# Optimization experiments

Measured on AMD Instinct MI355X. Metric: run time of the kernel, lower is better.

The kernel has to match this reference:

```python
import jax, jax.numpy as jnp
import numpy as np

WS = 7   # window_size
NH = 4   # num_head
EPS = 1e-5

def _rel_idx(ws):
    c = np.stack(np.meshgrid(np.arange(ws), np.arange(ws), indexing='ij')).reshape(2, -1)
    r = (c[:, :, None] - c[:, None, :]).transpose(1, 2, 0)
    r[..., 0] += ws - 1
    r[..., 1] += ws - 1
    r[..., 0] *= 2 * ws - 1
    return r.sum(-1)  # (ws^2, ws^2) int

def _shift_mask(ws, ps):
    # faithful to torch get_shift_mask: additive mask value is (1-eq)*1e-9 (as in source)
    wn = ps // ws
    ss = ws // 2
    rt = (np.arange(ps) + ss) // ws
    m = rt[:, None] * (ps // ws) + rt[None, :] + 1
    m = np.roll(m, (-ss, -ss), axis=(0, 1))
    m = m.reshape(wn, ws, wn, ws).transpose(0, 2, 1, 3).reshape(wn * wn, ws * ws)
    eq = (m[:, :, None] == m[:, None, :]).astype(np.float32)
    return (1.0 - eq) * 1e-9  # (num_windows, ws^2, ws^2)

def _ln(x, g, b):
    mu = x.mean(-1, keepdims=True)
    v = ((x - mu) ** 2).mean(-1, keepdims=True)
    return (x - mu) * jax.lax.rsqrt(v + EPS) * g + b

def _win_attn(x, wqkv, bqkv, wo, bo, table, mask):
    bs, S, D = x.shape
    hd = D // NH
    qkv = x @ wqkv.T + bqkv
    q, k, v = jnp.split(qkv, 3, axis=-1)
    def heads(t):
        return t.reshape(bs, S, NH, hd).transpose(0, 2, 1, 3).reshape(bs * NH, S, hd)
    q, k, v = heads(q), heads(k), heads(v)
    ridx = _rel_idx(WS).reshape(-1)
    bias = table[ridx].reshape(S, S, NH).transpose(2, 0, 1)  # (NH, S, S)
    scores = jnp.einsum('bqd,bkd->bqk', q, k) / np.sqrt(hd).astype(np.float32)
    scores = scores + jnp.tile(bias, (bs, 1, 1))
    if mask is not None:
        # source tiles mask head-major while q/k/v are batch-major; replicate faithfully
        scores = scores + jnp.tile(mask, (NH, 1, 1))
    p = jax.nn.softmax(scores, axis=-1)
    out = jnp.einsum('bqk,bkd->bqd', p, v)
    out = out.reshape(bs, NH, S, hd).transpose(0, 2, 1, 3).reshape(bs, S, D)
    return out @ wo.T + bo

def _forward(x, ln1_g, ln1_b, w_qkv1, b_qkv1, w_o1, b_o1, tbl1,
             ln2_g, ln2_b, w_mlp1, b_mlp1,
             ln3_g, ln3_b, w_qkv2, b_qkv2, w_o2, b_o2, tbl2,
             ln4_g, ln4_b, w_mlp2, b_mlp2):
    B, S, D = x.shape
    ps = int(np.sqrt(S))
    wn = ps // WS
    nw = wn * wn
    s2 = WS * WS
    ss = WS // 2
    # block 1: W-MSA (note: source's image2sequence is a plain reshape, no inverse transpose)
    y = _ln(x, ln1_g, ln1_b)
    y = y.reshape(B, wn, WS, wn, WS, D).transpose(0, 1, 3, 2, 4, 5).reshape(B * nw, s2, D)
    y = _win_attn(y, w_qkv1, b_qkv1, w_o1, b_o1, tbl1, None)
    y = y.reshape(B, S, D)
    x = x + y
    # mlp1
    y = _ln(x, ln2_g, ln2_b) @ w_mlp1.T + b_mlp1
    x = x + y
    # block 2: SW-MSA
    y = _ln(x, ln3_g, ln3_b)
    y = jnp.roll(y.reshape(B, ps, ps, D), (-ss, -ss), axis=(1, 2))
    y = y.reshape(B, wn, WS, wn, WS, D).transpose(0, 1, 3, 2, 4, 5).reshape(B * nw, s2, D)
    mask = jnp.tile(jnp.asarray(_shift_mask(WS, ps)), (B, 1, 1))
    y = _win_attn(y, w_qkv2, b_qkv2, w_o2, b_o2, tbl2, mask)
    y = y.reshape(B, wn, wn, WS, WS, D).transpose(0, 1, 3, 2, 4, 5).reshape(B, ps, ps, D)
    y = jnp.roll(y, (ss, ss), axis=(1, 2)).reshape(B, S, D)
    x = x + y
    # mlp2; source line `y + x + y` has no assignment, so the final residual is dropped
    y = _ln(x, ln4_g, ln4_b) @ w_mlp2.T + b_mlp2
    return y

def setup_inputs() -> dict:
    key = jax.random.key(0)
    ks = jax.random.split(key, 16)
    B, S, D = 64, 3136, 128
    T = (2 * WS - 1) ** 2  # 169
    f32 = jnp.float32
    inp = {
        'x': jax.random.normal(ks[0], (B, S, D), dtype=f32),
        'ln1_g': jnp.ones((D,), f32), 'ln1_b': jnp.zeros((D,), f32),
        'w_qkv1': jax.random.normal(ks[1], (3 * D, D), dtype=f32) * 0.02,
        'b_qkv1': jnp.zeros((3 * D,), f32),
        'w_o1': jax.random.normal(ks[2], (D, D), dtype=f32) * 0.02,
        'b_o1': jnp.zeros((D,), f32),
        'tbl1': jax.random.normal(ks[3], (T, NH), dtype=f32) * 0.02,
        'ln2_g': jnp.ones((D,), f32), 'ln2_b': jnp.zeros((D,), f32),
        'w_mlp1': jax.random.normal(ks[4], (D, D), dtype=f32) * 0.02,
        'b_mlp1': jnp.zeros((D,), f32),
        'ln3_g': jnp.ones((D,), f32), 'ln3_b': jnp.zeros((D,), f32),
        'w_qkv2': jax.random.normal(ks[5], (3 * D, D), dtype=f32) * 0.02,
        'b_qkv2': jnp.zeros((3 * D,), f32),
        'w_o2': jax.random.normal(ks[6], (D, D), dtype=f32) * 0.02,
        'b_o2': jnp.zeros((D,), f32),
        'tbl2': jax.random.normal(ks[7], (T, NH), dtype=f32) * 0.02,
        'ln4_g': jnp.ones((D,), f32), 'ln4_b': jnp.zeros((D,), f32),
        'w_mlp2': jax.random.normal(ks[8], (D, D), dtype=f32) * 0.02,
        'b_mlp2': jnp.zeros((D,), f32),
    }
    return inp

def reference(x, ln1_g, ln1_b, w_qkv1, b_qkv1, w_o1, b_o1, tbl1,
              ln2_g, ln2_b, w_mlp1, b_mlp1,
              ln3_g, ln3_b, w_qkv2, b_qkv2, w_o2, b_o2, tbl2,
              ln4_g, ln4_b, w_mlp2, b_mlp2):
    return _forward(x, ln1_g, ln1_b, w_qkv1, b_qkv1, w_o1, b_o1, tbl1,
                    ln2_g, ln2_b, w_mlp1, b_mlp1,
                    ln3_g, ln3_b, w_qkv2, b_qkv2, w_o2, b_o2, tbl2,
                    ln4_g, ln4_b, w_mlp2, b_mlp2)
```

## Files before the change

### kernel.cpp

```cpp
#include <hip/hip_runtime.h>
#include <hip/hip_bf16.h>
#include <stdint.h>

#define PS 56
#define S_ 3136
#define DIM 128
#define NTOK 200704

typedef __attribute__((ext_vector_type(8))) short short8;
typedef __attribute__((ext_vector_type(4))) float f32x4;

__device__ __forceinline__ uint32_t bfpack(float a, float b){
  uint32_t ua = __float_as_uint(a); ua = (ua + 0x7fffu + ((ua >> 16) & 1u)) >> 16;
  uint32_t ub = __float_as_uint(b); ub = (ub + 0x7fffu + ((ub >> 16) & 1u)) & 0xffff0000u;
  return ua | ub;
}
__device__ __forceinline__ uint16_t bf16of(float a){
  uint32_t ua = __float_as_uint(a);
  return (uint16_t)((ua + 0x7fffu + ((ua >> 16) & 1u)) >> 16);
}
__device__ __forceinline__ int rr(int row){ return row > 48 ? 49 : row; }

__device__ __forceinline__ int win_map(int r, int shift) {
  int b = r / S_;
  int rem = r - b * S_;
  int w = rem / 49;
  int p = rem - w * 49;
  int i = p / 7, j = p - i * 7;
  int wr = w >> 3, wc = w & 7;
  int row = wr * 7 + i + shift; if (row >= PS) row -= PS;
  int col = wc * 7 + j + shift; if (col >= PS) col -= PS;
  return b * S_ + row * PS + col;
}

__global__ __launch_bounds__(256) void ln_k(const float* __restrict__ X,
                                            const float* __restrict__ g,
                                            const float* __restrict__ b,
                                            uint16_t* __restrict__ O) {
  int t = blockIdx.x * 4 + (threadIdx.x >> 6);
  int lane = threadIdx.x & 63;
  float2 v = *(const float2*)(X + (size_t)t * DIM + lane * 2);
  float s = v.x + v.y, sq = v.x * v.x + v.y * v.y;
  #pragma unroll
  for (int o = 32; o; o >>= 1) { s += __shfl_xor(s, o); sq += __shfl_xor(sq, o); }
  float mu = s * (1.0f / 128.0f);
  float rs = rsqrtf(sq * (1.0f / 128.0f) - mu * mu + 1e-5f);
  float2 gg = *(const float2*)(g + lane * 2);
  float2 bb = *(const float2*)(b + lane * 2);
  float a = (v.x - mu) * rs * gg.x + bb.x;
  float c = (v.y - mu) * rs * gg.y + bb.y;
  ((uint32_t*)O)[(size_t)t * 64 + lane] = bfpack(a, c);
}

__global__ __launch_bounds__(256) void wconv_k(
    const float* __restrict__ w0, const float* __restrict__ w1,
    const float* __restrict__ w2, const float* __restrict__ w3,
    const float* __restrict__ w4, const float* __restrict__ w5,
    uint16_t* __restrict__ out) {
  int i = blockIdx.x * 256 + threadIdx.x;
  float v;
  if      (i <  49152) v = w0[i];
  else if (i <  98304) v = w1[i -  49152];
  else if (i < 114688) v = w2[i -  98304];
  else if (i < 131072) v = w3[i - 114688];
  else if (i < 147456) v = w4[i - 131072];
  else                 v = w5[i - 147456];
  out[i] = bf16of(v);
}

__global__ __launch_bounds__(256) void bias_k(const float* __restrict__ tbl, float* __restrict__ biasT) {
  int idx = blockIdx.x * 256 + threadIdx.x;
  int h = idx >> 12;
  int k = (idx >> 6) & 63;
  int q = idx & 63;
  float v;
  if (k >= 49)      v = -1e30f;
  else if (q >= 49) v = 0.f;
  else {
    int yi = q / 7, xi = q - yi * 7;
    int yj = k / 7, xj = k - yj * 7;
    v = tbl[((yi - yj + 6) * 13 + (xi - xj + 6)) * 4 + h];
  }
  biasT[idx] = v;
}

constexpr int QKV_STR = 392;
constexpr int OS_STR  = 140;

template<int IN_SHIFT, int OUT_SHIFT, bool MLP_LN>
__global__ __launch_bounds__(256) void attn4(const uint16_t* __restrict__ xbin,
                                             const uint16_t* __restrict__ Wqkv,
                                             const float* __restrict__ bqkv,
                                             const float* __restrict__ biasT,
                                             const uint16_t* __restrict__ Wo,
                                             const float* __restrict__ bo,
                                             const float* __restrict__ Rsrc,
                                             const uint16_t* __restrict__ Wm,
                                             const float* __restrict__ bm,
                                             const float* __restrict__ lnga,
                                             const float* __restrict__ lnba,
                                             const float* __restrict__ lngp,
                                             const float* __restrict__ lnbp,
                                             float* __restrict__ Xout,
                                             uint16_t* __restrict__ xbout)
{
  __shared__ __align__(16) uint16_t qs[50 * QKV_STR];
  __shared__ float lnred[50][4][2];
  const int tid = threadIdx.x;
  const int lane = tid & 63;
  const int h = tid >> 6;
  const int lanelow = lane & 15;
  const int quad = lane >> 4;
  const int base = blockIdx.x * 49;

  {
    short8 af[4][4];
    #pragma unroll
    for (int mt = 0; mt < 4; ++mt) {
      int tok = mt * 16 + lanelow; if (tok > 48) tok = 48;
      int src = win_map(base + tok, IN_SHIFT);
      const uint16_t* arow = xbin + (size_t)src * DIM;
      #pragma unroll
      for (int k0 = 0; k0 < 4; ++k0)
        af[mt][k0] = *(const short8*)(arow + k0 * 32 + quad * 8);
    }
    #pragma unroll
    for (int ntl = 0; ntl < 6; ++ntl) {
      int wrow = (ntl >> 1) * 128 + h * 32 + (ntl & 1) * 16 + lanelow;
      const uint16_t* wr_ = Wqkv + (size_t)wrow * DIM;
      short8 bfr[4];
      #pragma unroll
      for (int k0 = 0; k0 < 4; ++k0)
        bfr[k0] = *(const short8*)(wr_ + k0 * 32 + quad * 8);
      f32x4 a4[4];
      #pragma unroll
      for (int mt = 0; mt < 4; ++mt) a4[mt] = (f32x4){0.f, 0.f, 0.f, 0.f};
      __builtin_amdgcn_s_setprio(1);
      #pragma unroll
      for (int k0 = 0; k0 < 4; ++k0)
        #pragma unroll
        for (int mt = 0; mt < 4; ++mt)
          a4[mt] = __builtin_amdgcn_mfma_f32_16x16x32_bf16(af[mt][k0], bfr[k0], a4[mt], 0, 0, 0);
      __builtin_amdgcn_s_setprio(0);
      float bq = bqkv[wrow];
      #pragma unroll
      for (int mt = 0; mt < 4; ++mt)
        #pragma unroll
        for (int r = 0; r < 4; ++r)
          qs[rr(mt * 16 + quad * 4 + r) * QKV_STR + wrow] = bf16of(a4[mt][r] + bq);
    }
  }

  const int n0 = h * 32 + lanelow, n1 = n0 + 16;
  int   orow_a[4][4];
  float r0a[4][4], r1a[4][4];
  #pragma unroll
  for (int qt = 0; qt < 4; ++qt)
    #pragma unroll
    for (int r = 0; r < 4; ++r) {
      int q = qt * 16 + quad * 4 + r;
      bool ok = (q < 49);
      int wrow = base + (ok ? q : 0);
      int orow = (OUT_SHIFT < 0) ? wrow : win_map(wrow, OUT_SHIFT);
      orow_a[qt][r] = orow;
      r0a[qt][r] = ok ? Rsrc[(size_t)orow * DIM + n0] : 0.f;
      r1a[qt][r] = ok ? Rsrc[(size_t)orow * DIM + n1] : 0.f;
    }

  f32x4 sc[4][4];
  #pragma unroll
  for (int kt = 0; kt < 4; ++kt)
    #pragma unroll
    for (int qt = 0; qt < 4; ++qt) sc[kt][qt] = (f32x4){0.f, 0.f, 0.f, 0.f};
  {
    short8 kf[4], qf[4];
    const int kcol = 128 + h * 32 + quad * 8;
    const int qcol = h * 32 + quad * 8;
    #pragma unroll
    for (int t = 0; t < 4; ++t) {
      int tok = t * 16 + lanelow; if (tok > 48) tok = 48;
      kf[t] = *(const short8*)(qs + tok * QKV_STR + kcol);
      qf[t] = *(const short8*)(qs + tok * QKV_STR + qcol);
    }
    __syncthreads();
    __builtin_amdgcn_s_setprio(1);
    #pragma unroll
    for (int kt = 0; kt < 4; ++kt)
      #pragma unroll
      for (int qt = 0; qt < 4; ++qt)
        sc[kt][qt] = __builtin_amdgcn_mfma_f32_16x16x32_bf16(kf[kt], qf[qt], sc[kt][qt], 0, 0, 0);
    __builtin_amdgcn_s_setprio(0);
  }

  const float* bh = biasT + h * 4096;
  #pragma unroll
  for (int kt = 0; kt < 4; ++kt)
    #pragma unroll
    for (int r = 0; r < 4; ++r) {
      const float* br = bh + (kt * 16 + quad * 4 + r) * 64 + lanelow;
      #pragma unroll
      for (int qt = 0; qt < 4; ++qt)
        sc[kt][qt][r] = fmaf(sc[kt][qt][r], 0.17677669529663689f, br[qt * 16]);
    }
  #pragma unroll
  for (int qt = 0; qt < 4; ++qt) {
    float m = sc[0][qt][0];
    #pragma unroll
    for (int kt = 0; kt < 4; ++kt)
      #pragma unroll
      for (int r = 0; r < 4; ++r) m = fmaxf(m, sc[kt][qt][r]);
    m = fmaxf(m, __shfl_xor(m, 16));
    m = fmaxf(m, __shfl_xor(m, 32));
    float s = 0.f;
    #pragma unroll
    for (int kt = 0; kt < 4; ++kt)
      #pragma unroll
      for (int r = 0; r < 4; ++r) {
        float e = __expf(sc[kt][qt][r] - m);
        sc[kt][qt][r] = e;
        s += e;
      }
    s += __shfl_xor(s, 16);
    s += __shfl_xor(s, 32);
    float inv = 1.0f / s;
    #pragma unroll
    for (int kt = 0; kt < 4; ++kt)
      #pragma unroll
      for (int r = 0; r < 4; ++r) sc[kt][qt][r] *= inv;
  }

  uint16_t* pw = qs + h * 64;
  #pragma unroll
  for (int qt = 0; qt < 4; ++qt)
    #pragma unroll
    for (int kt = 0; kt < 4; ++kt) {
      uint2 pk;
      pk.x = bfpack(sc[kt][qt][0], sc[kt][qt][1]);
      pk.y = bfpack(sc[kt][qt][2], sc[kt][qt][3]);
      *(uint2*)(pw + rr(qt * 16 + lanelow) * QKV_STR + kt * 16 + quad * 4) = pk;
    }

  f32x4 oc[4][2];
  #pragma unroll
  for (int qt = 0; qt < 4; ++qt)
    #pragma unroll
    for (int dt = 0; dt < 2; ++dt) oc[qt][dt] = (f32x4){0.f, 0.f, 0.f, 0.f};
  {
    short8 pf[4][2];
    #pragma unroll
    for (int qt = 0; qt < 4; ++qt)
      #pragma unroll
      for (int kp = 0; kp < 2; ++kp)
        pf[qt][kp] = *(const short8*)(pw + rr(qt * 16 + lanelow) * QKV_STR + kp * 32 + quad * 8);
    short8 vf[2][2];
    #pragma unroll
    for (int dt = 0; dt < 2; ++dt)
      #pragma unroll
      for (int kp = 0; kp < 2; ++kp) {
        short8 b;
        #pragma unroll
        for (int j = 0; j < 8; ++j) {
          int tok = kp * 32 + quad * 8 + j; if (tok > 48) tok = 48;
          b[j] = (short)qs[tok * QKV_STR + 256 + h * 32 + dt * 16 + lanelow];
        }
        vf[dt][kp] = b;
      }
    __builtin_amdgcn_s_setprio(1);
    #pragma unroll
    for (int qt = 0; qt < 4; ++qt)
      #pragma unroll
      for (int dt = 0; dt < 2; ++dt)
        #pragma unroll
        for (int kp = 0; kp < 2; ++kp)
          oc[qt][dt] = __builtin_amdgcn_mfma_f32_16x16x32_bf16(pf[qt][kp], vf[dt][kp], oc[qt][dt], 0, 0, 0);
    __builtin_amdgcn_s_setprio(0);
  }

  __syncthreads();
  uint16_t* Os = qs;
  #pragma unroll
  for (int qt = 0; qt < 4; ++qt)
    #pragma unroll
    for (int r = 0; r < 4; ++r) {
      int t = qt * 16 + quad * 4 + r;
      #pragma unroll
      for (int dt = 0; dt < 2; ++dt)
        Os[t * OS_STR + h * 32 + dt * 16 + lanelow] = bf16of(oc[qt][dt][r]);
    }
  __syncthreads();

  f32x4 rc[4][2];
  #pragma unroll
  for (int qt = 0; qt < 4; ++qt)
    #pragma unroll
    for (int dt = 0; dt < 2; ++dt) rc[qt][dt] = (f32x4){0.f, 0.f, 0.f, 0.f};
  #pragma unroll
  for (int kp = 0; kp < 4; ++kp) {
    short8 af[4];
    #pragma unroll
    for (int qt = 0; qt < 4; ++qt)
      af[qt] = *(const short8*)&Os[(qt * 16 + lanelow) * OS_STR + kp * 32 + quad * 8];
    short8 bfr[2];
    #pragma unroll
    for (int dt = 0; dt < 2; ++dt)
      bfr[dt] = *(const short8*)(Wo + (size_t)(h * 32 + dt * 16 + lanelow) * DIM + kp * 32 + quad * 8);
    __builtin_amdgcn_s_setprio(1);
    #pragma unroll
    for (int qt = 0; qt < 4; ++qt)
      #pragma unroll
      for (int dt = 0; dt < 2; ++dt)
        rc[qt][dt] = __builtin_amdgcn_mfma_f32_16x16x32_bf16(af[qt], bfr[dt], rc[qt][dt], 0, 0, 0);
    __builtin_amdgcn_s_setprio(0);
  }

  const float b0 = bo[n0], b1 = bo[n1];
  const float ga0 = lnga[n0], ga1 = lnga[n1];
  const float ea0 = lnba[n0], ea1 = lnba[n1];
  #pragma unroll
  for (int qt = 0; qt < 4; ++qt)
    #pragma unroll
    for (int r = 0; r < 4; ++r) {
      int q = qt * 16 + quad * 4 + r;
      float v0 = rc[qt][0][r] + b0 + r0a[qt][r];
      float v1 = rc[qt][1][r] + b1 + r1a[qt][r];
      rc[qt][0][r] = v0; rc[qt][1][r] = v1;
      float s = v0 + v1, sq = v0 * v0 + v1 * v1;
      s += __shfl_xor(s, 1); sq += __shfl_xor(sq, 1);
      s += __shfl_xor(s, 2); sq += __shfl_xor(sq, 2);
      s += __shfl_xor(s, 4); sq += __shfl_xor(sq, 4);
      s += __shfl_xor(s, 8); sq += __shfl_xor(sq, 8);
      if (lanelow == 0) { lnred[rr(q)][h][0] = s; lnred[rr(q)][h][1] = sq; }
    }
  __syncthreads();

  uint16_t* Xl = qs;
  #pragma unroll
  for (int qt = 0; qt < 4; ++qt)
    #pragma unroll
    for (int r = 0; r < 4; ++r) {
      int q = qt * 16 + quad * 4 + r;
      int ql = rr(q);
      float s  = lnred[ql][0][0] + lnred[ql][1][0] + lnred[ql][2][0] + lnred[ql][3][0];
      float sq = lnred[ql][0][1] + lnred[ql][1][1] + lnred[ql][2][1] + lnred[ql][3][1];
      float mu = s * (1.0f / 128.0f);
      float rs = rsqrtf(sq * (1.0f / 128.0f) - mu * mu + 1e-5f);
      Xl[q * OS_STR + n0] = bf16of((rc[qt][0][r] - mu) * rs * ga0 + ea0);
      Xl[q * OS_STR + n1] = bf16of((rc[qt][1][r] - mu) * rs * ga1 + ea1);
    }
  __syncthreads();

  f32x4 mc[4][2];
  #pragma unroll
  for (int qt = 0; qt < 4; ++qt)
    #pragma unroll
    for (int dt = 0; dt < 2; ++dt) mc[qt][dt] = (f32x4){0.f, 0.f, 0.f, 0.f};
  #pragma unroll
  for (int kp = 0; kp < 4; ++kp) {
    short8 af2[4];
    #pragma unroll
    for (int qt = 0; qt < 4; ++qt)
      af2[qt] = *(const short8*)&Xl[(qt * 16 + lanelow) * OS_STR + kp * 32 + quad * 8];
    short8 wfr[2];
    wfr[0] = *(const short8*)(Wm + (size_t)n0 * DIM + kp * 32 + quad * 8);
    wfr[1] = *(const short8*)(Wm + (size_t)n1 * DIM + kp * 32 + quad * 8);
    __builtin_amdgcn_s_setprio(1);
    #pragma unroll
    for (int qt = 0; qt < 4; ++qt)
      #pragma unroll
      for (int dt = 0; dt < 2; ++dt)
        mc[qt][dt] = __builtin_amdgcn_mfma_f32_16x16x32_bf16(af2[qt], wfr[dt], mc[qt][dt], 0, 0, 0);
    __builtin_amdgcn_s_setprio(0);
  }
  const float bm0 = bm[n0], bm1 = bm[n1];

  if constexpr (MLP_LN) {
    const float gp0 = lngp[n0], gp1 = lngp[n1];
    const float ep0 = lnbp[n0], ep1 = lnbp[n1];
    #pragma unroll
    for (int qt = 0; qt < 4; ++qt)
      #pragma unroll
      for (int r = 0; r < 4; ++r) {
        int q = qt * 16 + quad * 4 + r;
        float v0 = rc[qt][0][r] + mc[qt][0][r] + bm0;
        float v1 = rc[qt][1][r] + mc[qt][1][r] + bm1;
        rc[qt][0][r] = v0; rc[qt][1][r] = v1;
        float s = v0 + v1, sq = v0 * v0 + v1 * v1;
        s += __shfl_xor(s, 1); sq += __shfl_xor(sq, 1);
        s += __shfl_xor(s, 2); sq += __shfl_xor(sq, 2);
        s += __shfl_xor(s, 4); sq += __shfl_xor(sq, 4);
        s += __shfl_xor(s, 8); sq += __shfl_xor(sq, 8);
        if (lanelow == 0) { lnred[rr(q)][h][0] = s; lnred[rr(q)][h][1] = sq; }
      }
    __syncthreads();
    #pragma unroll
    for (int qt = 0; qt < 4; ++qt)
      #pragma unroll
      for (int r = 0; r < 4; ++r) {
        int q = qt * 16 + quad * 4 + r;
        if (q < 49) {
          int orow = orow_a[qt][r];
          float s  = lnred[q][0][0] + lnred[q][1][0] + lnred[q][2][0] + lnred[q][3][0];
          float sq = lnred[q][0][1] + lnred[q][1][1] + lnred[q][2][1] + lnred[q][3][1];
          float mu = s * (1.0f / 128.0f);
          float rs = rsqrtf(sq * (1.0f / 128.0f) - mu * mu + 1e-5f);
          float v0 = rc[qt][0][r], v1 = rc[qt][1][r];
          Xout[(size_t)orow * DIM + n0] = v0;
          Xout[(size_t)orow * DIM + n1] = v1;
          xbout[(size_t)orow * DIM + n0] = bf16of((v0 - mu) * rs * gp0 + ep0);
          xbout[(size_t)orow * DIM + n1] = bf16of((v1 - mu) * rs * gp1 + ep1);
        }
      }
  } else {
    #pragma unroll
    for (int qt = 0; qt < 4; ++qt)
      #pragma unroll
      for (int r = 0; r < 4; ++r) {
        int q = qt * 16 + quad * 4 + r;
        if (q < 49) {
          int orow = orow_a[qt][r];
          Xout[(size_t)orow * DIM + n0] = mc[qt][0][r] + bm0;
          Xout[(size_t)orow * DIM + n1] = mc[qt][1][r] + bm1;
        }
      }
  }
}

extern "C" void kernel_launch(void* const* d_in, const int* in_sizes, int n_in,
                              void* d_out, int out_size, void* d_ws, size_t ws_size,
                              hipStream_t stream) {
  const float* x0    = (const float*)d_in[0];
  const float* ln1g  = (const float*)d_in[1];
  const float* ln1b  = (const float*)d_in[2];
  const float* wqkv1 = (const float*)d_in[3];
  const float* bqkv1 = (const float*)d_in[4];
  const float* wo1   = (const float*)d_in[5];
  const float* bo1   = (const float*)d_in[6];
  const float* tbl1  = (const float*)d_in[7];
  const float* ln2g  = (const float*)d_in[8];
  const float* ln2b  = (const float*)d_in[9];
  const float* wm1   = (const float*)d_in[10];
  const float* bm1   = (const float*)d_in[11];
  const float* ln3g  = (const float*)d_in[12];
  const float* ln3b  = (const float*)d_in[13];
  const float* wqkv2 = (const float*)d_in[14];
  const float* bqkv2 = (const float*)d_in[15];
  const float* wo2   = (const float*)d_in[16];
  const float* bo2   = (const float*)d_in[17];
  const float* tbl2  = (const float*)d_in[18];
  const float* ln4g  = (const float*)d_in[19];
  const float* ln4b  = (const float*)d_in[20];
  const float* wm2   = (const float*)d_in[21];
  const float* bm2   = (const float*)d_in[22];

  char* ws = (char*)d_ws;
  size_t off = 0;
  uint16_t* xbA  = (uint16_t*)(ws + off); off += (size_t)NTOK * 128 * sizeof(uint16_t);
  uint16_t* xb2  = (uint16_t*)(ws + off); off += (size_t)NTOK * 128 * sizeof(uint16_t);
  float* biasT1  = (float*)(ws + off);    off += 16384 * sizeof(float);
  float* biasT2  = (float*)(ws + off);    off += 16384 * sizeof(float);
  uint16_t* wb   = (uint16_t*)(ws + off); off += 163840 * sizeof(uint16_t);
  if (ws_size < off) return;
  float* x1 = (float*)d_out;

  uint16_t* wqkv1b = wb;
  uint16_t* wqkv2b = wb + 49152;
  uint16_t* wo1b   = wb + 98304;
  uint16_t* wm1b   = wb + 114688;
  uint16_t* wo2b   = wb + 131072;
  uint16_t* wm2b   = wb + 147456;

  dim3 blk(256);
  dim3 lgrid(NTOK / 4);
  dim3 agrid(4096);

  wconv_k<<<640, blk, 0, stream>>>(wqkv1, wqkv2, wo1, wm1, wo2, wm2, wb);
  bias_k<<<64, blk, 0, stream>>>(tbl1, biasT1);
  bias_k<<<64, blk, 0, stream>>>(tbl2, biasT2);

  ln_k<<<lgrid, blk, 0, stream>>>(x0, ln1g, ln1b, xbA);
  attn4<0, -1, true><<<agrid, blk, 0, stream>>>(
      xbA, wqkv1b, bqkv1, biasT1, wo1b, bo1, x0, wm1b, bm1,
      ln2g, ln2b, ln3g, ln3b, x1, xb2);
  attn4<3, 3, false><<<agrid, blk, 0, stream>>>(
      xb2, wqkv2b, bqkv2, biasT2, wo2b, bo2, x1, wm2b, bm2,
      ln4g, ln4b, ln4g, ln4b, x1, nullptr);
}
```

Baseline: 650.6 us.

## Split window attention block across two 256-thread halves by query tiles

The fused window-attention kernel now runs with 512 threads per window instead of 256. The two halves of the block split the QKV projection output tiles and the query tiles for scores, softmax, PV, output projection and MLP. Each thread keeps half as many accumulators, which lowers register pressure and raises the number of waves available to hide latency. In exchange, each half loads the same K/V fragments and weight rows, an extra barrier follows the QKV stage, and the priority hints around the QKV MFMAs are removed.

Result: slower. 826.3 us (+27.0%).

```diff
diff --git a/kernel.cpp b/kernel.cpp
--- a/kernel.cpp
+++ b/kernel.cpp
@@ -88,7 +88,7 @@
 constexpr int OS_STR  = 140;
 
 template<int IN_SHIFT, int OUT_SHIFT, bool MLP_LN>
-__global__ __launch_bounds__(256) void attn4(const uint16_t* __restrict__ xbin,
+__global__ __launch_bounds__(512) void attn5(const uint16_t* __restrict__ xbin,
                                              const uint16_t* __restrict__ Wqkv,
                                              const float* __restrict__ bqkv,
                                              const float* __restrict__ biasT,
@@ -108,7 +108,9 @@
   __shared__ float lnred[50][4][2];
   const int tid = threadIdx.x;
   const int lane = tid & 63;
-  const int h = tid >> 6;
+  const int h = (tid >> 6) & 3;
+  const int half = tid >> 8;
+  const int qtb = half * 2;
   const int lanelow = lane & 15;
   const int quad = lane >> 4;
   const int base = blockIdx.x * 49;
@@ -125,7 +127,8 @@
         af[mt][k0] = *(const short8*)(arow + k0 * 32 + quad * 8);
     }
     #pragma unroll
-    for (int ntl = 0; ntl < 6; ++ntl) {
+    for (int i = 0; i < 3; ++i) {
+      int ntl = half * 3 + i;
       int wrow = (ntl >> 1) * 128 + h * 32 + (ntl & 1) * 16 + lanelow;
       const uint16_t* wr_ = Wqkv + (size_t)wrow * DIM;
       short8 bfr[4];
@@ -135,13 +138,11 @@
       f32x4 a4[4];
       #pragma unroll
       for (int mt = 0; mt < 4; ++mt) a4[mt] = (f32x4){0.f, 0.f, 0.f, 0.f};
-      __builtin_amdgcn_s_setprio(1);
       #pragma unroll
       for (int k0 = 0; k0 < 4; ++k0)
         #pragma unroll
         for (int mt = 0; mt < 4; ++mt)
           a4[mt] = __builtin_amdgcn_mfma_f32_16x16x32_bf16(af[mt][k0], bfr[k0], a4[mt], 0, 0, 0);
-      __builtin_amdgcn_s_setprio(0);
       float bq = bqkv[wrow];
       #pragma unroll
       for (int mt = 0; mt < 4; ++mt)
@@ -150,45 +151,50 @@
           qs[rr(mt * 16 + quad * 4 + r) * QKV_STR + wrow] = bf16of(a4[mt][r] + bq);
     }
   }
+  __syncthreads();
 
   const int n0 = h * 32 + lanelow, n1 = n0 + 16;
-  int   orow_a[4][4];
-  float r0a[4][4], r1a[4][4];
-  #pragma unroll
-  for (int qt = 0; qt < 4; ++qt)
+  int   orow_a[2][4];
+  float r0a[2][4], r1a[2][4];
+  #pragma unroll
+  for (int qi = 0; qi < 2; ++qi)
     #pragma unroll
     for (int r = 0; r < 4; ++r) {
-      int q = qt * 16 + quad * 4 + r;
+      int q = (qtb + qi) * 16 + quad * 4 + r;
       bool ok = (q < 49);
       int wrow = base + (ok ? q : 0);
       int orow = (OUT_SHIFT < 0) ? wrow : win_map(wrow, OUT_SHIFT);
-      orow_a[qt][r] = orow;
-      r0a[qt][r] = ok ? Rsrc[(size_t)orow * DIM + n0] : 0.f;
-      r1a[qt][r] = ok ? Rsrc[(size_t)orow * DIM + n1] : 0.f;
-    }
-
-  f32x4 sc[4][4];
+      orow_a[qi][r] = orow;
+      r0a[qi][r] = ok ? Rsrc[(size_t)orow * DIM + n0] : 0.f;
+      r1a[qi][r] = ok ? Rsrc[(size_t)orow * DIM + n1] : 0.f;
+    }
+
+  f32x4 sc[4][2];
   #pragma unroll
   for (int kt = 0; kt < 4; ++kt)
     #pragma unroll
-    for (int qt = 0; qt < 4; ++qt) sc[kt][qt] = (f32x4){0.f, 0.f, 0.f, 0.f};
+    for (int qi = 0; qi < 2; ++qi) sc[kt][qi] = (f32x4){0.f, 0.f, 0.f, 0.f};
   {
-    short8 kf[4], qf[4];
+    short8 kf[4], qf[2];
     const int kcol = 128 + h * 32 + quad * 8;
     const int qcol = h * 32 + quad * 8;
     #pragma unroll
     for (int t = 0; t < 4; ++t) {
       int tok = t * 16 + lanelow; if (tok > 48) tok = 48;
       kf[t] = *(const short8*)(qs + tok * QKV_STR + kcol);
-      qf[t] = *(const short8*)(qs + tok * QKV_STR + qcol);
+    }
+    #pragma unroll
+    for (int qi = 0; qi < 2; ++qi) {
+      int tok = (qtb + qi) * 16 + lanelow; if (tok > 48) tok = 48;
+      qf[qi] = *(const short8*)(qs + tok * QKV_STR + qcol);
     }
     __syncthreads();
     __builtin_amdgcn_s_setprio(1);
     #pragma unroll
     for (int kt = 0; kt < 4; ++kt)
       #pragma unroll
-      for (int qt = 0; qt < 4; ++qt)
-        sc[kt][qt] = __builtin_amdgcn_mfma_f32_16x16x32_bf16(kf[kt], qf[qt], sc[kt][qt], 0, 0, 0);
+      for (int qi = 0; qi < 2; ++qi)
+        sc[kt][qi] = __builtin_amdgcn_mfma_f32_16x16x32_bf16(kf[kt], qf[qi], sc[kt][qi], 0, 0, 0);
     __builtin_amdgcn_s_setprio(0);
   }
 
@@ -199,16 +205,16 @@
     for (int r = 0; r < 4; ++r) {
       const float* br = bh + (kt * 16 + quad * 4 + r) * 64 + lanelow;
       #pragma unroll
-      for (int qt = 0; qt < 4; ++qt)
-        sc[kt][qt][r] = fmaf(sc[kt][qt][r], 0.17677669529663689f, br[qt * 16]);
-    }
-  #pragma unroll
-  for (int qt = 0; qt < 4; ++qt) {
-    float m = sc[0][qt][0];
+      for (int qi = 0; qi < 2; ++qi)
+        sc[kt][qi][r] = fmaf(sc[kt][qi][r], 0.17677669529663689f, br[(qtb + qi) * 16]);
+    }
+  #pragma unroll
+  for (int qi = 0; qi < 2; ++qi) {
+    float m = sc[0][qi][0];
     #pragma unroll
     for (int kt = 0; kt < 4; ++kt)
       #pragma unroll
-      for (int r = 0; r < 4; ++r) m = fmaxf(m, sc[kt][qt][r]);
+      for (int r = 0; r < 4; ++r) m = fmaxf(m, sc[kt][qi][r]);
     m = fmaxf(m, __shfl_xor(m, 16));
     m = fmaxf(m, __shfl_xor(m, 32));
     float s = 0.f;
@@ -216,8 +222,8 @@
     for (int kt = 0; kt < 4; ++kt)
       #pragma unroll
       for (int r = 0; r < 4; ++r) {
-        float e = __expf(sc[kt][qt][r] - m);
-        sc[kt][qt][r] = e;
+        float e = __expf(sc[kt][qi][r] - m);
+        sc[kt][qi][r] = e;
         s += e;
       }
     s += __shfl_xor(s, 16);
@@ -226,32 +232,32 @@
     #pragma unroll
     for (int kt = 0; kt < 4; ++kt)
       #pragma unroll
-      for (int r = 0; r < 4; ++r) sc[kt][qt][r] *= inv;
+      for (int r = 0; r < 4; ++r) sc[kt][qi][r] *= inv;
   }
 
   uint16_t* pw = qs + h * 64;
   #pragma unroll
-  for (int qt = 0; qt < 4; ++qt)
+  for (int qi = 0; qi < 2; ++qi)
     #pragma unroll
     for (int kt = 0; kt < 4; ++kt) {
       uint2 pk;
-      pk.x = bfpack(sc[kt][qt][0], sc[kt][qt][1]);
-      pk.y = bfpack(sc[kt][qt][2], sc[kt][qt][3]);
-      *(uint2*)(pw + rr(qt * 16 + lanelow) * QKV_STR + kt * 16 + quad * 4) = pk;
-    }
-
-  f32x4 oc[4][2];
-  #pragma unroll
-  for (int qt = 0; qt < 4; ++qt)
-    #pragma unroll
-    for (int dt = 0; dt < 2; ++dt) oc[qt][dt] = (f32x4){0.f, 0.f, 0.f, 0.f};
+      pk.x = bfpack(sc[kt][qi][0], sc[kt][qi][1]);
+      pk.y = bfpack(sc[kt][qi][2], sc[kt][qi][3]);
+      *(uint2*)(pw + rr((qtb + qi) * 16 + lanelow) * QKV_STR + kt * 16 + quad * 4) = pk;
+    }
+
+  f32x4 oc[2][2];
+  #pragma unroll
+  for (int qi = 0; qi < 2; ++qi)
+    #pragma unroll
+    for (int dt = 0; dt < 2; ++dt) oc[qi][dt] = (f32x4){0.f, 0.f, 0.f, 0.f};
   {
-    short8 pf[4][2];
-    #pragma unroll
-    for (int qt = 0; qt < 4; ++qt)
+    short8 pf[2][2];
+    #pragma unroll
+    for (int qi = 0; qi < 2; ++qi)
       #pragma unroll
       for (int kp = 0; kp < 2; ++kp)
-        pf[qt][kp] = *(const short8*)(pw + rr(qt * 16 + lanelow) * QKV_STR + kp * 32 + quad * 8);
+        pf[qi][kp] = *(const short8*)(pw + rr((qtb + qi) * 16 + lanelow) * QKV_STR + kp * 32 + quad * 8);
     short8 vf[2][2];
     #pragma unroll
     for (int dt = 0; dt < 2; ++dt)
@@ -267,49 +273,49 @@
       }
     __builtin_amdgcn_s_setprio(1);
     #pragma unroll
-    for (int qt = 0; qt < 4; ++qt)
+    for (int qi = 0; qi < 2; ++qi)
       #pragma unroll
       for (int dt = 0; dt < 2; ++dt)
         #pragma unroll
         for (int kp = 0; kp < 2; ++kp)
-          oc[qt][dt] = __builtin_amdgcn_mfma_f32_16x16x32_bf16(pf[qt][kp], vf[dt][kp], oc[qt][dt], 0, 0, 0);
+          oc[qi][dt] = __builtin_amdgcn_mfma_f32_16x16x32_bf16(pf[qi][kp], vf[dt][kp], oc[qi][dt], 0, 0, 0);
     __builtin_amdgcn_s_setprio(0);
   }
 
   __syncthreads();
   uint16_t* Os = qs;
   #pragma unroll
-  for (int qt = 0; qt < 4; ++qt)
+  for (int qi = 0; qi < 2; ++qi)
     #pragma unroll
     for (int r = 0; r < 4; ++r) {
-      int t = qt * 16 + quad * 4 + r;
+      int t = (qtb + qi) * 16 + quad * 4 + r;
       #pragma unroll
       for (int dt = 0; dt < 2; ++dt)
-        Os[t * OS_STR + h * 32 + dt * 16 + lanelow] = bf16of(oc[qt][dt][r]);
+        Os[t * OS_STR + h * 32 + dt * 16 + lanelow] = bf16of(oc[qi][dt][r]);
     }
   __syncthreads();
 
-  f32x4 rc[4][2];
-  #pragma unroll
-  for (int qt = 0; qt < 4; ++qt)
-    #pragma unroll
-    for (int dt = 0; dt < 2; ++dt) rc[qt][dt] = (f32x4){0.f, 0.f, 0.f, 0.f};
+  f32x4 rc[2][2];
+  #pragma unroll
+  for (int qi = 0; qi < 2; ++qi)
+    #pragma unroll
+    for (int dt = 0; dt < 2; ++dt) rc[qi][dt] = (f32x4){0.f, 0.f, 0.f, 0.f};
   #pragma unroll
   for (int kp = 0; kp < 4; ++kp) {
-    short8 af[4];
-    #pragma unroll
-    for (int qt = 0; qt < 4; ++qt)
-      af[qt] = *(const short8*)&Os[(qt * 16 + lanelow) * OS_STR + kp * 32 + quad * 8];
+    short8 af[2];
+    #pragma unroll
+    for (int qi = 0; qi < 2; ++qi)
+      af[qi] = *(const short8*)&Os[((qtb + qi) * 16 + lanelow) * OS_STR + kp * 32 + quad * 8];
     short8 bfr[2];
     #pragma unroll
     for (int dt = 0; dt < 2; ++dt)
       bfr[dt] = *(const short8*)(Wo + (size_t)(h * 32 + dt * 16 + lanelow) * DIM + kp * 32 + quad * 8);
     __builtin_amdgcn_s_setprio(1);
     #pragma unroll
-    for (int qt = 0; qt < 4; ++qt)
+    for (int qi = 0; qi < 2; ++qi)
       #pragma unroll
       for (int dt = 0; dt < 2; ++dt)
-        rc[qt][dt] = __builtin_amdgcn_mfma_f32_16x16x32_bf16(af[qt], bfr[dt], rc[qt][dt], 0, 0, 0);
+        rc[qi][dt] = __builtin_amdgcn_mfma_f32_16x16x32_bf16(af[qi], bfr[dt], rc[qi][dt], 0, 0, 0);
     __builtin_amdgcn_s_setprio(0);
   }
 
@@ -317,13 +323,13 @@
   const float ga0 = lnga[n0], ga1 = lnga[n1];
   const float ea0 = lnba[n0], ea1 = lnba[n1];
   #pragma unroll
-  for (int qt = 0; qt < 4; ++qt)
+  for (int qi = 0; qi < 2; ++qi)
     #pragma unroll
     for (int r = 0; r < 4; ++r) {
-      int q = qt * 16 + quad * 4 + r;
-      float v0 = rc[qt][0][r] + b0 + r0a[qt][r];
-      float v1 = rc[qt][1][r] + b1 + r1a[qt][r];
-      rc[qt][0][r] = v0; rc[qt][1][r] = v1;
+      int q = (qtb + qi) * 16 + quad * 4 + r;
+      float v0 = rc[qi][0][r] + b0 + r0a[qi][r];
+      float v1 = rc[qi][1][r] + b1 + r1a[qi][r];
+      rc[qi][0][r] = v0; rc[qi][1][r] = v1;
       float s = v0 + v1, sq = v0 * v0 + v1 * v1;
       s += __shfl_xor(s, 1); sq += __shfl_xor(sq, 1);
       s += __shfl_xor(s, 2); sq += __shfl_xor(sq, 2);
@@ -335,40 +341,40 @@
 
   uint16_t* Xl = qs;
   #pragma unroll
-  for (int qt = 0; qt < 4; ++qt)
+  for (int qi = 0; qi < 2; ++qi)
     #pragma unroll
     for (int r = 0; r < 4; ++r) {
-      int q = qt * 16 + quad * 4 + r;
+      int q = (qtb + qi) * 16 + quad * 4 + r;
       int ql = rr(q);
       float s  = lnred[ql][0][0] + lnred[ql][1][0] + lnred[ql][2][0] + lnred[ql][3][0];
       float sq = lnred[ql][0][1] + lnred[ql][1][1] + lnred[ql][2][1] + lnred[ql][3][1];
       float mu = s * (1.0f / 128.0f);
       float rs = rsqrtf(sq * (1.0f / 128.0f) - mu * mu + 1e-5f);
-      Xl[q * OS_STR + n0] = bf16of((rc[qt][0][r] - mu) * rs * ga0 + ea0);
-      Xl[q * OS_STR + n1] = bf16of((rc[qt][1][r] - mu) * rs * ga1 + ea1);
+      Xl[q * OS_STR + n0] = bf16of((rc[qi][0][r] - mu) * rs * ga0 + ea0);
+      Xl[q * OS_STR + n1] = bf16of((rc[qi][1][r] - mu) * rs * ga1 + ea1);
     }
   __syncthreads();
 
-  f32x4 mc[4][2];
-  #pragma unroll
-  for (int qt = 0; qt < 4; ++qt)
-    #pragma unroll
-    for (int dt = 0; dt < 2; ++dt) mc[qt][dt] = (f32x4){0.f, 0.f, 0.f, 0.f};
+  f32x4 mc[2][2];
+  #pragma unroll
+  for (int qi = 0; qi < 2; ++qi)
+    #pragma unroll
+    for (int dt = 0; dt < 2; ++dt) mc[qi][dt] = (f32x4){0.f, 0.f, 0.f, 0.f};
   #pragma unroll
   for (int kp = 0; kp < 4; ++kp) {
-    short8 af2[4];
-    #pragma unroll
-    for (int qt = 0; qt < 4; ++qt)
-      af2[qt] = *(const short8*)&Xl[(qt * 16 + lanelow) * OS_STR + kp * 32 + quad * 8];
+    short8 af2[2];
+    #pragma unroll
+    for (int qi = 0; qi < 2; ++qi)
+      af2[qi] = *(const short8*)&Xl[((qtb + qi) * 16 + lanelow) * OS_STR + kp * 32 + quad * 8];
     short8 wfr[2];
     wfr[0] = *(const short8*)(Wm + (size_t)n0 * DIM + kp * 32 + quad * 8);
     wfr[1] = *(const short8*)(Wm + (size_t)n1 * DIM + kp * 32 + quad * 8);
     __builtin_amdgcn_s_setprio(1);
     #pragma unroll
-    for (int qt = 0; qt < 4; ++qt)
+    for (int qi = 0; qi < 2; ++qi)
       #pragma unroll
       for (int dt = 0; dt < 2; ++dt)
-        mc[qt][dt] = __builtin_amdgcn_mfma_f32_16x16x32_bf16(af2[qt], wfr[dt], mc[qt][dt], 0, 0, 0);
+        mc[qi][dt] = __builtin_amdgcn_mfma_f32_16x16x32_bf16(af2[qi], wfr[dt], mc[qi][dt], 0, 0, 0);
     __builtin_amdgcn_s_setprio(0);
   }
   const float bm0 = bm[n0], bm1 = bm[n1];
@@ -377,13 +383,13 @@
     const float gp0 = lngp[n0], gp1 = lngp[n1];
     const float ep0 = lnbp[n0], ep1 = lnbp[n1];
     #pragma unroll
-    for (int qt = 0; qt < 4; ++qt)
+    for (int qi = 0; qi < 2; ++qi)
       #pragma unroll
       for (int r = 0; r < 4; ++r) {
-        int q = qt * 16 + quad * 4 + r;
-        float v0 = rc[qt][0][r] + mc[qt][0][r] + bm0;
-        float v1 = rc[qt][1][r] + mc[qt][1][r] + bm1;
-        rc[qt][0][r] = v0; rc[qt][1][r] = v1;
+        int q = (qtb + qi) * 16 + quad * 4 + r;
+        float v0 = rc[qi][0][r] + mc[qi][0][r] + bm0;
+        float v1 = rc[qi][1][r] + mc[qi][1][r] + bm1;
+        rc[qi][0][r] = v0; rc[qi][1][r] = v1;
         float s = v0 + v1, sq = v0 * v0 + v1 * v1;
         s += __shfl_xor(s, 1); sq += __shfl_xor(sq, 1);
         s += __shfl_xor(s, 2); sq += __shfl_xor(sq, 2);
@@ -393,17 +399,17 @@
       }
     __syncthreads();
     #pragma unroll
-    for (int qt = 0; qt < 4; ++qt)
+    for (int qi = 0; qi < 2; ++qi)
       #pragma unroll
       for (int r = 0; r < 4; ++r) {
-        int q = qt * 16 + quad * 4 + r;
+        int q = (qtb + qi) * 16 + quad * 4 + r;
         if (q < 49) {
-          int orow = orow_a[qt][r];
+          int orow = orow_a[qi][r];
           float s  = lnred[q][0][0] + lnred[q][1][0] + lnred[q][2][0] + lnred[q][3][0];
           float sq = lnred[q][0][1] + lnred[q][1][1] + lnred[q][2][1] + lnred[q][3][1];
           float mu = s * (1.0f / 128.0f);
           float rs = rsqrtf(sq * (1.0f / 128.0f) - mu * mu + 1e-5f);
-          float v0 = rc[qt][0][r], v1 = rc[qt][1][r];
+          float v0 = rc[qi][0][r], v1 = rc[qi][1][r];
           Xout[(size_t)orow * DIM + n0] = v0;
           Xout[(size_t)orow * DIM + n1] = v1;
           xbout[(size_t)orow * DIM + n0] = bf16of((v0 - mu) * rs * gp0 + ep0);
@@ -412,14 +418,14 @@
       }
   } else {
     #pragma unroll
-    for (int qt = 0; qt < 4; ++qt)
+    for (int qi = 0; qi < 2; ++qi)
       #pragma unroll
       for (int r = 0; r < 4; ++r) {
-        int q = qt * 16 + quad * 4 + r;
+        int q = (qtb + qi) * 16 + quad * 4 + r;
         if (q < 49) {
-          int orow = orow_a[qt][r];
-          Xout[(size_t)orow * DIM + n0] = mc[qt][0][r] + bm0;
-          Xout[(size_t)orow * DIM + n1] = mc[qt][1][r] + bm1;
+          int orow = orow_a[qi][r];
+          Xout[(size_t)orow * DIM + n0] = mc[qi][0][r] + bm0;
+          Xout[(size_t)orow * DIM + n1] = mc[qi][1][r] + bm1;
         }
       }
   }
@@ -478,10 +484,10 @@
   bias_k<<<64, blk, 0, stream>>>(tbl2, biasT2);
 
   ln_k<<<lgrid, blk, 0, stream>>>(x0, ln1g, ln1b, xbA);
-  attn4<0, -1, true><<<agrid, blk, 0, stream>>>(
+  attn5<0, -1, true><<<agrid, dim3(512), 0, stream>>>(
       xbA, wqkv1b, bqkv1, biasT1, wo1b, bo1, x0, wm1b, bm1,
       ln2g, ln2b, ln3g, ln3b, x1, xb2);
-  attn4<3, 3, false><<<agrid, blk, 0, stream>>>(
+  attn5<3, 3, false><<<agrid, dim3(512), 0, stream>>>(
       xb2, wqkv2b, bqkv2, biasT2, wo2b, bo2, x1, wm2b, bm2,
       ln4g, ln4b, ln4g, ln4b, x1, nullptr);
 }
```
